# Performance work log

Hardware: AMD Instinct MI355X
Metric: run time of the kernel (lower is better)

Reference implementation:

```python
import jax, jax.numpy as jnp
import numpy as np

NUM_HEADS = 4
OUTPUT_DIM = 64


def setup_inputs() -> dict:
    key = jax.random.key(0)
    k1, k2, k3 = jax.random.split(key, 3)
    B, N, F = 8, 2048, 256
    features = jax.random.normal(k1, (B, N, F), dtype=jnp.float32)
    adj_matrix = jax.random.uniform(k2, (B, N, N), dtype=jnp.float32)
    # learned params (glorot-ish scale)
    kernel = jax.random.normal(k3, (F, OUTPUT_DIM * NUM_HEADS), dtype=jnp.float32) * (1.0 / np.sqrt(F))
    bias = jnp.zeros((OUTPUT_DIM * NUM_HEADS,), dtype=jnp.float32)
    return {"features": features, "adj_matrix": adj_matrix, "kernel": kernel, "bias": bias}


def reference(features, adj_matrix, kernel, bias):
    B, N, F = features.shape
    H, D = NUM_HEADS, OUTPUT_DIM
    Wh = jnp.matmul(features, kernel)                 # [B, N, H*D]
    Whh = Wh.reshape(B, N, H, D)                      # [B, N, H, D]
    # per-node, per-head score: inner product Wh1 @ Wh2 = ||Wh||^2
    e = jnp.sum(Whh * Whh, axis=-1)                   # [B, N, H]
    attention = jax.nn.softmax(e, axis=1)             # softmax over nodes
    attention = jnp.mean(attention, axis=2)           # head mean -> [B, N]
    # adjacency mask (broadcast column score over neighbors)
    A = attention[:, :, None] * adj_matrix            # [B, N, N]
    out = jnp.matmul(A, Wh) + bias                    # [B, N, H*D]
    return jax.nn.relu(out)
```

## Files before the change

### kernel.cpp

```cpp
#include <hip/hip_runtime.h>
#include <hip/hip_bf16.h>

#define BATCH 8
#define NNODE 2048
#define FDIM 256
#define HD 256
#define NH 4
#define MROWS (BATCH*NNODE)

typedef float f32x4 __attribute__((ext_vector_type(4)));
typedef short s16x8 __attribute__((ext_vector_type(8)));
typedef unsigned short ushort_t;

#define MFMA __builtin_amdgcn_mfma_f32_16x16x32_bf16
#define SCHED0() __builtin_amdgcn_sched_barrier(0)
#define SBAR() __builtin_amdgcn_s_barrier()

__device__ __forceinline__ void split2(float f, ushort_t& h, ushort_t& l) {
    unsigned u = __builtin_bit_cast(unsigned, f);
    h = (ushort_t)(u >> 16);
    float fh = __builtin_bit_cast(float, u & 0xffff0000u);
    float lo = f - fh;
    l = (ushort_t)(__builtin_bit_cast(unsigned, lo) >> 16);
}

#define GLOAD16(gp, lp) __builtin_amdgcn_global_load_lds( \
    (const __attribute__((address_space(1))) void*)(gp),  \
    (__attribute__((address_space(3))) void*)(lp), 16, 0, 0)

__global__ __launch_bounds__(256) void wprep_kernel(
    const float* __restrict__ Wm,
    ushort_t* __restrict__ wt_hi, ushort_t* __restrict__ wt_lo)
{
    const int nn = blockIdx.x, k = threadIdx.x;
    ushort_t h, l;
    split2(Wm[(size_t)k * HD + nn], h, l);
    wt_hi[nn * FDIM + k] = h;
    wt_lo[nn * FDIM + k] = l;
}

__global__ __launch_bounds__(256, 4) void gemm1_kernel(
    const float* __restrict__ features,
    const ushort_t* __restrict__ wt_hi,
    const ushort_t* __restrict__ wt_lo,
    ushort_t* __restrict__ WhT_hi,
    ushort_t* __restrict__ WhT_lo,
    float* __restrict__ e_out)
{
    __shared__ __align__(16) ushort_t Ah[64 * 64];
    __shared__ __align__(16) ushort_t Al[64 * 64];
    __shared__ __align__(16) ushort_t Bh[64 * 64];
    __shared__ __align__(16) ushort_t Bl[64 * 64];
    __shared__ float red[64][2];

    const int tid = threadIdx.x, lane = tid & 63, w = tid >> 6;
    const int wr = w >> 1, wc = w & 1;
    const int row0 = blockIdx.x * 64;
    const int head = blockIdx.y;
    const int col0 = head * 64;

    const float* Ab = features + (size_t)row0 * FDIM;
    const ushort_t* Bhg = wt_hi + (size_t)col0 * FDIM;
    const ushort_t* Blg = wt_lo + (size_t)col0 * FDIM;

    const int sr0 = tid >> 3;
    const int sg8 = tid & 7;
    const int bc = (lane >> 3);
    const int bs = lane & 7;

    f32x4 ar[4];
    f32x4 acc[2][2];
    #pragma unroll
    for (int m = 0; m < 2; ++m)
        #pragma unroll
        for (int n = 0; n < 2; ++n) acc[m][n] = (f32x4)0.f;

    #define G1_LOADA(K0) do {                                                  \
        _Pragma("unroll")                                                      \
        for (int i = 0; i < 2; ++i) {                                          \
            const int r = sr0 + 32 * i;                                        \
            ar[2*i]   = *(const f32x4*)&Ab[(size_t)r * FDIM + (K0) + sg8 * 8]; \
            ar[2*i+1] = *(const f32x4*)&Ab[(size_t)r * FDIM + (K0) + sg8 * 8 + 4]; \
        }                                                                      \
    } while (0)

    #define G1_STAGEA() do {                                                   \
        _Pragma("unroll")                                                      \
        for (int i = 0; i < 2; ++i) {                                          \
            const int r = sr0 + 32 * i;                                        \
            s16x8 vh, vl; ushort_t hh, ll;                                     \
            _Pragma("unroll")                                                  \
            for (int j = 0; j < 4; ++j) {                                      \
                split2(ar[2*i][j], hh, ll);  vh[j] = (short)hh; vl[j] = (short)ll; \
            }                                                                  \
            _Pragma("unroll")                                                  \
            for (int j = 0; j < 4; ++j) {                                      \
                split2(ar[2*i+1][j], hh, ll); vh[4+j] = (short)hh; vl[4+j] = (short)ll; \
            }                                                                  \
            const int off = r * 64 + ((sg8 ^ (r & 7)) << 3);                   \
            *(s16x8*)&Ah[off] = vh; *(s16x8*)&Al[off] = vl;                    \
        }                                                                      \
    } while (0)

    #define G1_STAGEB(K0) do {                                                 \
        _Pragma("unroll")                                                      \
        for (int qq = 0; qq < 2; ++qq) {                                       \
            const int q = w + qq * 4;                                          \
            const int c = q * 8 + bc;                                          \
            const int g = bs ^ (c & 7);                                        \
            GLOAD16(&Bhg[(size_t)c * FDIM + (K0) + g * 8], &Bh[q * 512]);      \
            GLOAD16(&Blg[(size_t)c * FDIM + (K0) + g * 8], &Bl[q * 512]);      \
        }                                                                      \
    } while (0)

    G1_LOADA(0);
    for (int t = 0; t < 4; ++t) {
        G1_STAGEB(t * 64);
        G1_STAGEA();
        if (t < 3) G1_LOADA((t + 1) * 64);
        if (t < 3) { asm volatile("s_waitcnt lgkmcnt(0) vmcnt(4)" ::: "memory"); }
        else       { asm volatile("s_waitcnt lgkmcnt(0) vmcnt(0)" ::: "memory"); }
        SCHED0(); SBAR(); SCHED0();
        #pragma unroll
        for (int kh = 0; kh < 2; ++kh) {
            const int kg = kh * 4 + (lane >> 4);
            s16x8 afh[2], afl[2], bfh[2], bfl[2];
            #pragma unroll
            for (int m = 0; m < 2; ++m) {
                const int r = wr * 32 + m * 16 + (lane & 15);
                const int off = r * 64 + ((kg ^ (r & 7)) << 3);
                afh[m] = *(const s16x8*)&Ah[off];
                afl[m] = *(const s16x8*)&Al[off];
            }
            #pragma unroll
            for (int n = 0; n < 2; ++n) {
                const int c = wc * 32 + n * 16 + (lane & 15);
                const int off = c * 64 + ((kg ^ (c & 7)) << 3);
                bfh[n] = *(const s16x8*)&Bh[off];
                bfl[n] = *(const s16x8*)&Bl[off];
            }
            #pragma unroll
            for (int m = 0; m < 2; ++m)
                #pragma unroll
                for (int n = 0; n < 2; ++n) {
                    acc[m][n] = MFMA(afh[m], bfh[n], acc[m][n], 0, 0, 0);
                    acc[m][n] = MFMA(afh[m], bfl[n], acc[m][n], 0, 0, 0);
                    acc[m][n] = MFMA(afl[m], bfh[n], acc[m][n], 0, 0, 0);
                }
        }
        SCHED0(); SBAR(); SCHED0();
    }

    #pragma unroll
    for (int m = 0; m < 2; ++m)
        #pragma unroll
        for (int j = 0; j < 4; ++j) {
            float p = acc[m][0][j] * acc[m][0][j] + acc[m][1][j] * acc[m][1][j];
            p += __shfl_xor(p, 1, 64);
            p += __shfl_xor(p, 2, 64);
            p += __shfl_xor(p, 4, 64);
            p += __shfl_xor(p, 8, 64);
            if ((lane & 15) == 0)
                red[wr * 32 + m * 16 + (lane >> 4) * 4 + j][wc] = p;
        }

    ushort_t* Th = Ah;
    ushort_t* Tl = Al;
    #pragma unroll
    for (int m = 0; m < 2; ++m)
        #pragma unroll
        for (int n = 0; n < 2; ++n)
            #pragma unroll
            for (int j = 0; j < 4; ++j) {
                const int rr = wr * 32 + m * 16 + (lane >> 4) * 4 + j;
                const int cc = wc * 32 + n * 16 + (lane & 15);
                const int ad = cc * 64 + ((((rr >> 3) ^ (cc & 7))) << 3) + (rr & 7);
                ushort_t hh, ll;
                split2(acc[m][n][j], hh, ll);
                Th[ad] = hh; Tl[ad] = ll;
            }
    __syncthreads();

    if (tid < 64) {
        const int rg = row0 + tid;
        e_out[((size_t)((rg >> 11) * NH + head)) * NNODE + (rg & 2047)] =
            red[tid][0] + red[tid][1];
    }
    const int bb = row0 >> 11, node0 = row0 & 2047;
    #pragma unroll
    for (int i = 0; i < 2; ++i) {
        const int gid = tid + 256 * i;
        const int c = gid >> 3, gr = gid & 7;
        const int ad = c * 64 + ((gr ^ (c & 7)) << 3);
        uint4 vh = *(const uint4*)&Th[ad];
        uint4 vl = *(const uint4*)&Tl[ad];
        const size_t o = ((size_t)bb * HD + col0 + c) * NNODE + node0 + gr * 8;
        *(uint4*)&WhT_hi[o] = vh;
        *(uint4*)&WhT_lo[o] = vl;
    }
}

__global__ __launch_bounds__(256) void sm_kernel(
    const float* __restrict__ e, float* __restrict__ ms)
{
    __shared__ float red[8];
    const int bh = blockIdx.x, tid = threadIdx.x;
    const int lane = tid & 63, w = tid >> 6;
    const float* row = e + (size_t)bh * NNODE;
    float mx = -3.0e38f;
    for (int n = tid; n < NNODE; n += 256) mx = fmaxf(mx, row[n]);
    #pragma unroll
    for (int off = 32; off; off >>= 1) mx = fmaxf(mx, __shfl_xor(mx, off, 64));
    if (lane == 0) red[w] = mx;
    __syncthreads();
    mx = fmaxf(fmaxf(red[0], red[1]), fmaxf(red[2], red[3]));
    float s = 0.f;
    for (int n = tid; n < NNODE; n += 256) s += expf(row[n] - mx);
    #pragma unroll
    for (int off = 32; off; off >>= 1) s += __shfl_xor(s, off, 64);
    if (lane == 0) red[4 + w] = s;
    __syncthreads();
    if (tid == 0) {
        ms[bh * 2] = mx;
        ms[bh * 2 + 1] = red[4] + red[5] + red[6] + red[7];
    }
}

__global__ __launch_bounds__(256) void att_kernel(
    const float* __restrict__ e, const float* __restrict__ ms,
    float* __restrict__ attv)
{
    const int i = blockIdx.x * 256 + threadIdx.x;
    const int b = i >> 11, n = i & 2047;
    float a = 0.f;
    #pragma unroll
    for (int h = 0; h < NH; ++h) {
        const int bh = b * NH + h;
        a += expf(e[(size_t)bh * NNODE + n] - ms[bh * 2]) / ms[bh * 2 + 1];
    }
    attv[i] = 0.25f * a;
}

__global__ __launch_bounds__(256, 2) void gemm2_kernel(
    const float* __restrict__ adj,
    const ushort_t* __restrict__ WhT_hi,
    const ushort_t* __restrict__ WhT_lo,
    const float* __restrict__ att,
    const float* __restrict__ bias,
    float* __restrict__ out)
{
    __shared__ __align__(16) ushort_t Ah[128 * 64];
    __shared__ __align__(16) ushort_t Al[128 * 64];
    __shared__ __align__(16) ushort_t Bh[2][64 * 64];
    __shared__ __align__(16) ushort_t Bl[2][64 * 64];

    const int tid = threadIdx.x, lane = tid & 63, w = tid >> 6;
    const int wr = w >> 1, wc = w & 1;
    const int b = blockIdx.z;
    const int row0 = blockIdx.x * 128, col0 = blockIdx.y * 64;

    const float* Ab = adj + (size_t)b * NNODE * NNODE + (size_t)row0 * NNODE;
    const ushort_t* Bhg = WhT_hi + ((size_t)b * HD + col0) * NNODE;
    const ushort_t* Blg = WhT_lo + ((size_t)b * HD + col0) * NNODE;

    const int sr0 = tid >> 3;
    const int sg8 = tid & 7;
    const int bc = lane >> 3, bs = lane & 7;

    f32x4 ar[8];
    f32x4 acc[4][2];
    #pragma unroll
    for (int m = 0; m < 4; ++m)
        #pragma unroll
        for (int n = 0; n < 2; ++n) acc[m][n] = (f32x4)0.f;

    #define G2_LOADA(K0) do {                                                   \
        _Pragma("unroll")                                                       \
        for (int i = 0; i < 4; ++i) {                                           \
            const int r = sr0 + 32 * i;                                         \
            ar[2*i]   = *(const f32x4*)&Ab[(size_t)r * NNODE + (K0) + sg8 * 8]; \
            ar[2*i+1] = *(const f32x4*)&Ab[(size_t)r * NNODE + (K0) + sg8 * 8 + 4]; \
        }                                                                       \
    } while (0)

    #define G2_STAGEA() do {                                                    \
        _Pragma("unroll")                                                       \
        for (int i = 0; i < 4; ++i) {                                           \
            const int r = sr0 + 32 * i;                                         \
            s16x8 vh, vl; ushort_t hh, ll;                                      \
            _Pragma("unroll")                                                   \
            for (int j = 0; j < 4; ++j) {                                       \
                split2(ar[2*i][j], hh, ll);  vh[j] = (short)hh; vl[j] = (short)ll; \
            }                                                                   \
            _Pragma("unroll")                                                   \
            for (int j = 0; j < 4; ++j) {                                       \
                split2(ar[2*i+1][j], hh, ll); vh[4+j] = (short)hh; vl[4+j] = (short)ll; \
            }                                                                   \
            const int off = r * 64 + ((sg8 ^ (r & 7)) << 3);                    \
            *(s16x8*)&Ah[off] = vh; *(s16x8*)&Al[off] = vl;                     \
        }                                                                       \
    } while (0)

    #define G2_STAGEB(BUF, K0) do {                                             \
        _Pragma("unroll")                                                       \
        for (int qq = 0; qq < 2; ++qq) {                                        \
            const int q = w + qq * 4;                                           \
            const int c = q * 8 + bc;                                           \
            const int g = bs ^ (c & 7);                                         \
            GLOAD16(&Bhg[(size_t)c * NNODE + (K0) + g * 8], &Bh[BUF][q * 512]); \
            GLOAD16(&Blg[(size_t)c * NNODE + (K0) + g * 8], &Bl[BUF][q * 512]); \
        }                                                                       \
    } while (0)

    #define G2_COMPUTE(BUF) do {                                                \
        _Pragma("unroll")                                                       \
        for (int kh = 0; kh < 2; ++kh) {                                        \
            const int kg = kh * 4 + (lane >> 4);                                \
            s16x8 afh[4], afl[4], bfh[2], bfl[2];                               \
            _Pragma("unroll")                                                   \
            for (int m = 0; m < 4; ++m) {                                       \
                const int r = wr * 64 + m * 16 + (lane & 15);                   \
                const int off = r * 64 + ((kg ^ (r & 7)) << 3);                 \
                afh[m] = *(const s16x8*)&Ah[off];                               \
                afl[m] = *(const s16x8*)&Al[off];                               \
            }                                                                   \
            _Pragma("unroll")                                                   \
            for (int n = 0; n < 2; ++n) {                                       \
                const int c = wc * 32 + n * 16 + (lane & 15);                   \
                const int off = c * 64 + ((kg ^ (c & 7)) << 3);                 \
                bfh[n] = *(const s16x8*)&Bh[BUF][off];                          \
                bfl[n] = *(const s16x8*)&Bl[BUF][off];                          \
            }                                                                   \
            _Pragma("unroll")                                                   \
            for (int m = 0; m < 4; ++m)                                         \
            _Pragma("unroll")                                                   \
            for (int n = 0; n < 2; ++n) {                                       \
                acc[m][n] = MFMA(afh[m], bfh[n], acc[m][n], 0, 0, 0);           \
                acc[m][n] = MFMA(afh[m], bfl[n], acc[m][n], 0, 0, 0);           \
                acc[m][n] = MFMA(afl[m], bfh[n], acc[m][n], 0, 0, 0);           \
            }                                                                   \
        }                                                                       \
    } while (0)

    G2_LOADA(0);
    G2_STAGEB(0, 0);
    G2_STAGEA();
    G2_LOADA(64);
    asm volatile("s_waitcnt lgkmcnt(0) vmcnt(8)" ::: "memory");
    SCHED0(); SBAR(); SCHED0();

    for (int t = 0; t < 32; ++t) {
        const int cur = t & 1;
        if (t < 31) G2_STAGEB(cur ^ 1, (t + 1) * 64);
        G2_COMPUTE(cur);
        if (t < 31) {
            SCHED0(); SBAR(); SCHED0();
            G2_STAGEA();
            if (t < 30) {
                G2_LOADA((t + 2) * 64);
                asm volatile("s_waitcnt lgkmcnt(0) vmcnt(8)" ::: "memory");
            } else {
                asm volatile("s_waitcnt lgkmcnt(0) vmcnt(0)" ::: "memory");
            }
            SCHED0(); SBAR(); SCHED0();
        }
    }

    const float* attb = att + (size_t)b * NNODE;
    #pragma unroll
    for (int n = 0; n < 2; ++n) {
        const int c = col0 + wc * 32 + n * 16 + (lane & 15);
        const float bv = bias[c];
        #pragma unroll
        for (int m = 0; m < 4; ++m)
            #pragma unroll
            for (int j = 0; j < 4; ++j) {
                const int row = row0 + wr * 64 + m * 16 + (lane >> 4) * 4 + j;
                out[((size_t)b * NNODE + row) * HD + c] =
                    fmaxf(fmaf(acc[m][n][j], attb[row], bv), 0.f);
            }
    }
}

extern "C" void kernel_launch(void* const* d_in, const int* in_sizes, int n_in,
                              void* d_out, int out_size, void* d_ws, size_t ws_size,
                              hipStream_t stream) {
    const float* features = (const float*)d_in[0];
    const float* adj      = (const float*)d_in[1];
    const float* Wm       = (const float*)d_in[2];
    const float* bias     = (const float*)d_in[3];
    float* out = (float*)d_out;

    ushort_t* WhT_hi = (ushort_t*)d_ws;
    ushort_t* WhT_lo = WhT_hi + (size_t)BATCH * HD * NNODE;
    ushort_t* wt_hi  = WhT_lo + (size_t)BATCH * HD * NNODE;
    ushort_t* wt_lo  = wt_hi + FDIM * HD;
    float* e    = (float*)(wt_lo + FDIM * HD);
    float* ms   = e + (size_t)BATCH * NH * NNODE;
    float* attv = ms + 64;

    wprep_kernel<<<HD, 256, 0, stream>>>(Wm, wt_hi, wt_lo);
    gemm1_kernel<<<dim3(MROWS / 64, NH), 256, 0, stream>>>(
        features, wt_hi, wt_lo, WhT_hi, WhT_lo, e);
    sm_kernel<<<BATCH * NH, 256, 0, stream>>>(e, ms);
    att_kernel<<<MROWS / 256, 256, 0, stream>>>(e, ms, attv);
    gemm2_kernel<<<dim3(NNODE / 128, HD / 64, BATCH), 256, 0, stream>>>(
        adj, WhT_hi, WhT_lo, attv, bias, out);
}
```

Measured before the change: 289.0 us.

## Load adjacency directly into MFMA registers and triple-buffer B tiles

The second GEMM no longer stages the fp32 adjacency tile through shared memory. Each wave loads its own 32 rows straight into MFMA operand layout and splits them into bf16 hi/lo pairs in registers. The B operand (Wh^T hi/lo) moves to a three-slot shared-memory ring, needing one barrier per k-step instead of two. MFMA blocks are wrapped in setprio, and a missing __syncthreads is added in the first kernel before reusing its shared buffers. The direct adjacency loads are less coalesced per row and raise register pressure, and correctness depends on the vmcnt count and the 3-buffer reuse distance.

```diff
diff --git a/kernel.cpp b/kernel.cpp
--- a/kernel.cpp
+++ b/kernel.cpp
@@ -164,6 +164,7 @@
                 red[wr * 32 + m * 16 + (lane >> 4) * 4 + j][wc] = p;
         }
 
+    __syncthreads();
     ushort_t* Th = Ah;
     ushort_t* Tl = Al;
     #pragma unroll
@@ -249,55 +250,54 @@
     const float* __restrict__ bias,
     float* __restrict__ out)
 {
-    __shared__ __align__(16) ushort_t Ah[128 * 64];
-    __shared__ __align__(16) ushort_t Al[128 * 64];
-    __shared__ __align__(16) ushort_t Bh[2][64 * 64];
-    __shared__ __align__(16) ushort_t Bl[2][64 * 64];
+    __shared__ __align__(16) ushort_t Bh[3][64 * 64];
+    __shared__ __align__(16) ushort_t Bl[3][64 * 64];
 
     const int tid = threadIdx.x, lane = tid & 63, w = tid >> 6;
-    const int wr = w >> 1, wc = w & 1;
     const int b = blockIdx.z;
     const int row0 = blockIdx.x * 128, col0 = blockIdx.y * 64;
 
-    const float* Ab = adj + (size_t)b * NNODE * NNODE + (size_t)row0 * NNODE;
     const ushort_t* Bhg = WhT_hi + ((size_t)b * HD + col0) * NNODE;
     const ushort_t* Blg = WhT_lo + ((size_t)b * HD + col0) * NNODE;
 
-    const int sr0 = tid >> 3;
-    const int sg8 = tid & 7;
+    const float* pA = adj + (size_t)b * NNODE * NNODE
+                    + (size_t)(row0 + w * 32 + (lane & 15)) * NNODE
+                    + ((lane >> 4) * 8);
+
     const int bc = lane >> 3, bs = lane & 7;
 
-    f32x4 ar[8];
-    f32x4 acc[4][2];
-    #pragma unroll
-    for (int m = 0; m < 4; ++m)
-        #pragma unroll
-        for (int n = 0; n < 2; ++n) acc[m][n] = (f32x4)0.f;
+    f32x4 ar[2][2][2];
+    s16x8 afh[2][2], afl[2][2];
+    f32x4 acc[2][4];
+    #pragma unroll
+    for (int m = 0; m < 2; ++m)
+        #pragma unroll
+        for (int n = 0; n < 4; ++n) acc[m][n] = (f32x4)0.f;
 
     #define G2_LOADA(K0) do {                                                   \
         _Pragma("unroll")                                                       \
-        for (int i = 0; i < 4; ++i) {                                           \
-            const int r = sr0 + 32 * i;                                         \
-            ar[2*i]   = *(const f32x4*)&Ab[(size_t)r * NNODE + (K0) + sg8 * 8]; \
-            ar[2*i+1] = *(const f32x4*)&Ab[(size_t)r * NNODE + (K0) + sg8 * 8 + 4]; \
+        for (int m = 0; m < 2; ++m)                                             \
+        _Pragma("unroll")                                                       \
+        for (int ks = 0; ks < 2; ++ks) {                                        \
+            ar[m][ks][0] = *(const f32x4*)&pA[(size_t)m * 16 * NNODE + (K0) + ks * 32]; \
+            ar[m][ks][1] = *(const f32x4*)&pA[(size_t)m * 16 * NNODE + (K0) + ks * 32 + 4]; \
         }                                                                       \
     } while (0)
 
-    #define G2_STAGEA() do {                                                    \
-        _Pragma("unroll")                                                       \
-        for (int i = 0; i < 4; ++i) {                                           \
-            const int r = sr0 + 32 * i;                                         \
-            s16x8 vh, vl; ushort_t hh, ll;                                      \
+    #define G2_CONVERT() do {                                                   \
+        _Pragma("unroll")                                                       \
+        for (int m = 0; m < 2; ++m)                                             \
+        _Pragma("unroll")                                                       \
+        for (int ks = 0; ks < 2; ++ks) {                                        \
+            ushort_t hh, ll;                                                    \
+            _Pragma("unroll")                                                   \
+            for (int h2 = 0; h2 < 2; ++h2)                                      \
             _Pragma("unroll")                                                   \
             for (int j = 0; j < 4; ++j) {                                       \
-                split2(ar[2*i][j], hh, ll);  vh[j] = (short)hh; vl[j] = (short)ll; \
+                split2(ar[m][ks][h2][j], hh, ll);                               \
+                afh[m][ks][h2 * 4 + j] = (short)hh;                             \
+                afl[m][ks][h2 * 4 + j] = (short)ll;                             \
             }                                                                   \
-            _Pragma("unroll")                                                   \
-            for (int j = 0; j < 4; ++j) {                                       \
-                split2(ar[2*i+1][j], hh, ll); vh[4+j] = (short)hh; vl[4+j] = (short)ll; \
-            }                                                                   \
-            const int off = r * 64 + ((sg8 ^ (r & 7)) << 3);                    \
-            *(s16x8*)&Ah[off] = vh; *(s16x8*)&Al[off] = vl;                     \
         }                                                                       \
     } while (0)
 
@@ -312,70 +312,60 @@
         }                                                                       \
     } while (0)
 
-    #define G2_COMPUTE(BUF) do {                                                \
-        _Pragma("unroll")                                                       \
-        for (int kh = 0; kh < 2; ++kh) {                                        \
-            const int kg = kh * 4 + (lane >> 4);                                \
-            s16x8 afh[4], afl[4], bfh[2], bfl[2];                               \
-            _Pragma("unroll")                                                   \
-            for (int m = 0; m < 4; ++m) {                                       \
-                const int r = wr * 64 + m * 16 + (lane & 15);                   \
-                const int off = r * 64 + ((kg ^ (r & 7)) << 3);                 \
-                afh[m] = *(const s16x8*)&Ah[off];                               \
-                afl[m] = *(const s16x8*)&Al[off];                               \
+    #define G2_COMPUTE(BHP, BLP) do {                                           \
+        _Pragma("unroll")                                                       \
+        for (int ks = 0; ks < 2; ++ks) {                                        \
+            const int kg = ks * 4 + (lane >> 4);                                \
+            s16x8 bfh[4], bfl[4];                                               \
+            _Pragma("unroll")                                                   \
+            for (int n = 0; n < 4; ++n) {                                       \
+                const int c = n * 16 + (lane & 15);                             \
+                const int off = c * 64 + ((kg ^ (c & 7)) << 3);                 \
+                bfh[n] = *(const s16x8*)&(BHP)[off];                            \
+                bfl[n] = *(const s16x8*)&(BLP)[off];                            \
             }                                                                   \
-            _Pragma("unroll")                                                   \
-            for (int n = 0; n < 2; ++n) {                                       \
-                const int c = wc * 32 + n * 16 + (lane & 15);                   \
-                const int off = c * 64 + ((kg ^ (c & 7)) << 3);                 \
-                bfh[n] = *(const s16x8*)&Bh[BUF][off];                          \
-                bfl[n] = *(const s16x8*)&Bl[BUF][off];                          \
+            __builtin_amdgcn_s_setprio(1);                                      \
+            _Pragma("unroll")                                                   \
+            for (int m = 0; m < 2; ++m)                                         \
+            _Pragma("unroll")                                                   \
+            for (int n = 0; n < 4; ++n) {                                       \
+                acc[m][n] = MFMA(afh[m][ks], bfh[n], acc[m][n], 0, 0, 0);       \
+                acc[m][n] = MFMA(afh[m][ks], bfl[n], acc[m][n], 0, 0, 0);       \
+                acc[m][n] = MFMA(afl[m][ks], bfh[n], acc[m][n], 0, 0, 0);       \
             }                                                                   \
-            _Pragma("unroll")                                                   \
-            for (int m = 0; m < 4; ++m)                                         \
-            _Pragma("unroll")                                                   \
-            for (int n = 0; n < 2; ++n) {                                       \
-                acc[m][n] = MFMA(afh[m], bfh[n], acc[m][n], 0, 0, 0);           \
-                acc[m][n] = MFMA(afh[m], bfl[n], acc[m][n], 0, 0, 0);           \
-                acc[m][n] = MFMA(afl[m], bfh[n], acc[m][n], 0, 0, 0);           \
-            }                                                                   \
+            __builtin_amdgcn_s_setprio(0);                                      \
         }                                                                       \
     } while (0)
 
+    G2_STAGEB(0, 0);
     G2_LOADA(0);
-    G2_STAGEB(0, 0);
-    G2_STAGEA();
-    G2_LOADA(64);
-    asm volatile("s_waitcnt lgkmcnt(0) vmcnt(8)" ::: "memory");
-    SCHED0(); SBAR(); SCHED0();
-
+
+    int cur = 0;
     for (int t = 0; t < 32; ++t) {
-        const int cur = t & 1;
-        if (t < 31) G2_STAGEB(cur ^ 1, (t + 1) * 64);
-        G2_COMPUTE(cur);
-        if (t < 31) {
-            SCHED0(); SBAR(); SCHED0();
-            G2_STAGEA();
-            if (t < 30) {
-                G2_LOADA((t + 2) * 64);
-                asm volatile("s_waitcnt lgkmcnt(0) vmcnt(8)" ::: "memory");
-            } else {
-                asm volatile("s_waitcnt lgkmcnt(0) vmcnt(0)" ::: "memory");
-            }
-            SCHED0(); SBAR(); SCHED0();
+        const int nxt = (cur == 2) ? 0 : cur + 1;
+        if (t < 31) G2_STAGEB(nxt, (t + 1) * 64);
+        G2_CONVERT();
+        if (t < 31) G2_LOADA((t + 1) * 64);
+        asm volatile("s_waitcnt vmcnt(12)" ::: "memory");
+        SCHED0(); SBAR(); SCHED0();
+        {
+            const ushort_t* bhp = &Bh[cur][0];
+            const ushort_t* blp = &Bl[cur][0];
+            G2_COMPUTE(bhp, blp);
         }
+        cur = nxt;
     }
 
     const float* attb = att + (size_t)b * NNODE;
     #pragma unroll
-    for (int n = 0; n < 2; ++n) {
-        const int c = col0 + wc * 32 + n * 16 + (lane & 15);
+    for (int n = 0; n < 4; ++n) {
+        const int c = col0 + n * 16 + (lane & 15);
         const float bv = bias[c];
         #pragma unroll
-        for (int m = 0; m < 4; ++m)
+        for (int m = 0; m < 2; ++m)
             #pragma unroll
             for (int j = 0; j < 4; ++j) {
-                const int row = row0 + wr * 64 + m * 16 + (lane >> 4) * 4 + j;
+                const int row = row0 + w * 32 + m * 16 + (lane >> 4) * 4 + j;
                 out[((size_t)b * NNODE + row) * HD + c] =
                     fmaxf(fmaf(acc[m][n][j], attb[row], bv), 0.f);
             }
```

Result: faster. 276.8 us (-4.2%).
